# Kernel optimization log

Hardware: AMD Instinct MI355X
Metric: run time of the kernel (lower is better)

## Reference

```python
import jax, jax.numpy as jnp
import numpy as np
import math

H = 8
D_MODEL = 512
D_K = D_MODEL // H
DIM_G = 64
WAVE_LEN = 1000.0


def box_relational_embedding(f_g):
    # f_g: [B, N, 4] -> [B, N, N, 64] trigonometric geometry embedding
    x_min, y_min, x_max, y_max = jnp.split(f_g, 4, axis=-1)  # each [B,N,1]
    cx = (x_min + x_max) * 0.5
    cy = (y_min + y_max) * 0.5
    w = x_max - x_min + 1.0
    h = y_max - y_min + 1.0
    # pairwise deltas: [B,N,1] vs [B,1,N] -> [B,N,N]
    cx_t = jnp.swapaxes(cx, 1, 2)  # [B,1,N]
    cy_t = jnp.swapaxes(cy, 1, 2)
    w_t = jnp.swapaxes(w, 1, 2)
    h_t = jnp.swapaxes(h, 1, 2)
    delta_x = jnp.log(jnp.maximum(jnp.abs((cx - cx_t) / w), 0.001))
    delta_y = jnp.log(jnp.maximum(jnp.abs((cy - cy_t) / h), 0.001))
    delta_w = jnp.log(w / w_t)
    delta_h = jnp.log(h / h_t)
    position_mat = jnp.stack([delta_x, delta_y, delta_w, delta_h], axis=-1)  # [B,N,N,4]
    feat_range = jnp.arange(DIM_G // 8, dtype=position_mat.dtype) / (DIM_G / 8)
    dim_mat = 1.0 / jnp.power(jnp.asarray(WAVE_LEN, position_mat.dtype), feat_range)  # [8]
    mul_mat = (100.0 * position_mat)[..., None] * dim_mat  # [B,N,N,4,8]
    B, N = position_mat.shape[0], position_mat.shape[1]
    mul_mat = mul_mat.reshape(B, N, N, -1)  # [B,N,N,32]
    return jnp.concatenate([jnp.sin(mul_mat), jnp.cos(mul_mat)], axis=-1)  # [B,N,N,64]


def setup_inputs() -> dict:
    key = jax.random.key(0)
    ks = jax.random.split(key, 16)
    B, N = 16, 256
    scale = 1.0 / math.sqrt(D_MODEL)
    inp = {
        'input_query': jax.random.normal(ks[0], (B, N, D_MODEL), jnp.float32),
        'input_key': jax.random.normal(ks[1], (B, N, D_MODEL), jnp.float32),
        'input_value': jax.random.normal(ks[2], (B, N, D_MODEL), jnp.float32),
        'input_box': jax.random.uniform(ks[3], (B, N, 4), jnp.float32),
        'mask': jnp.ones((B, N), jnp.int32),
        # projection weights stored as [d_in, d_out] (x @ W + b)
        'Wq': jax.random.normal(ks[4], (D_MODEL, D_MODEL), jnp.float32) * scale,
        'bq': jnp.zeros((D_MODEL,), jnp.float32),
        'Wk': jax.random.normal(ks[5], (D_MODEL, D_MODEL), jnp.float32) * scale,
        'bk': jnp.zeros((D_MODEL,), jnp.float32),
        'Wv': jax.random.normal(ks[6], (D_MODEL, D_MODEL), jnp.float32) * scale,
        'bv': jnp.zeros((D_MODEL,), jnp.float32),
        'Wo': jax.random.normal(ks[7], (D_MODEL, D_MODEL), jnp.float32) * scale,
        'bo': jnp.zeros((D_MODEL,), jnp.float32),
        # 8 geometric-bias heads: Linear(64 -> 1) each, stacked -> [H, 64], [H]
        'WG_w': jax.random.normal(ks[8], (H, DIM_G), jnp.float32) * (1.0 / math.sqrt(DIM_G)),
        'WG_b': jnp.zeros((H,), jnp.float32),
    }
    return inp


def reference(input_query, input_key, input_value, input_box, mask,
              Wq, bq, Wk, bk, Wv, bv, Wo, bo, WG_w, WG_b):
    B, N, _ = input_query.shape

    def proj(x, W, b):  # [B,N,D] -> [B,H,N,d_k]
        return (x @ W + b).reshape(B, N, H, D_K).transpose(0, 2, 1, 3)

    q = proj(input_query, Wq, bq)
    k = proj(input_key, Wk, bk)
    v = proj(input_value, Wv, bv)

    geo = box_relational_embedding(input_box)  # [B,N,N,64]
    # per-head geometric weights, ReLU'd: [B,H,N,N]
    w_g = jax.nn.relu(jnp.einsum('bnmg,hg->bhnm', geo, WG_w) + WG_b[None, :, None, None])

    scaled_dot = jnp.einsum('bhqd,bhkd->bhqk', q, k) / np.sqrt(D_K).astype(q.dtype)
    # mask: [B,N] keys -> [B,1,1,N], broadcast over heads and queries
    scaled_dot = jnp.where(mask[:, None, None, :] == 0, jnp.asarray(-1e9, scaled_dot.dtype), scaled_dot)
    w_mn = jax.nn.softmax(jnp.log(jnp.maximum(w_g, 1e-6)) + scaled_dot, axis=-1)
    # dropout is identity in eval mode
    out = jnp.einsum('bhqk,bhkd->bhqd', w_mn, v)  # [B,H,N,d_k]
    out = out.transpose(0, 2, 1, 3).reshape(B, N, H * D_K)
    return out @ Wo + bo
```

## Files before the change

### kernel.cpp

```cpp
#include <hip/hip_runtime.h>
#include <hip/hip_fp16.h>
#include <math.h>

#define Bv   16
#define Nv   256
#define Dv   512
#define Hv   8
#define MNv  4096

typedef __attribute__((ext_vector_type(8))) short bf16x8;
typedef __attribute__((ext_vector_type(4))) float f32x4;
typedef __fp16 fp16x8 __attribute__((ext_vector_type(8)));
typedef __fp16 fp16x2 __attribute__((ext_vector_type(2)));

__device__ __forceinline__ unsigned short f2bf(float f) {
    unsigned u = __float_as_uint(f);
    u = u + 0x7FFFu + ((u >> 16) & 1u);
    return (unsigned short)(u >> 16);
}
__device__ __forceinline__ void gload_lds16(const void* g, void* l) {
    __builtin_amdgcn_global_load_lds(
        (const __attribute__((address_space(1))) unsigned int*)g,
        (__attribute__((address_space(3))) unsigned int*)l, 16, 0, 0);
}

__device__ __forceinline__ void fast_sincos(float x, float* s, float* c) {
    const float rev = x * 0.15915494309189535f;
    const float fr  = rev - floorf(rev);
    *s = __builtin_amdgcn_sinf(fr);
    *c = __builtin_amdgcn_cosf(fr);
}
__device__ __forceinline__ float fast_log(float x) {
    return __builtin_amdgcn_logf(x) * 0.6931471805599453f;
}
__device__ __forceinline__ float fast_exp(float x) {
    return __builtin_amdgcn_exp2f(x * 1.4426950408889634f);
}

__global__ __launch_bounds__(256) void mega1_kernel(
    const float* __restrict__ box, const int* __restrict__ mask,
    const float* __restrict__ WGw, const float* __restrict__ WGb,
    __half* __restrict__ LB,
    const float* __restrict__ xq, const float* __restrict__ xk,
    const float* __restrict__ xv, unsigned short* __restrict__ Ab,
    const float* __restrict__ Wq, const float* __restrict__ Wk,
    const float* __restrict__ Wv, const float* __restrict__ Wo,
    const float* __restrict__ bq, const float* __restrict__ bk,
    const float* __restrict__ bv, const float* __restrict__ bo,
    unsigned short* __restrict__ Wt, float* __restrict__ biasStack)
{
    __shared__ __align__(16) char smraw[64 * 65 * 4];
    const int bid = blockIdx.x;
    const int t = threadIdx.x;

    if (bid < 4096) {
        unsigned short (*Lst)[264] = (unsigned short (*)[264])smraw;
        const int q = bid & 255;
        const int b = bid >> 8;
        const int w = t >> 6, lane = t & 63;
        const int n = lane & 15;
        const int quad = lane >> 4;

        const float4 bq_ = *(const float4*)(box + (b * Nv + q) * 4);
        const float cxq = (bq_.x + bq_.z) * 0.5f;
        const float cyq = (bq_.y + bq_.w) * 0.5f;
        const float wq  = bq_.z - bq_.x + 1.0f;
        const float hq  = bq_.w - bq_.y + 1.0f;

        union F16x8 { fp16x8 v; fp16x2 p[4]; };
        F16x8 Bs_, Bc_;
        Bs_.v = (fp16x8){}; Bc_.v = (fp16x8){};
        float bias_n = 0.0f;
        if (n < Hv) {
            bias_n = WGb[n];
#pragma unroll
            for (int jj = 0; jj < 4; ++jj) {
                Bs_.p[jj] = __builtin_amdgcn_cvt_pkrtz(WGw[n * 64 + quad * 8 + 2 * jj],
                                                       WGw[n * 64 + quad * 8 + 2 * jj + 1]);
                Bc_.p[jj] = __builtin_amdgcn_cvt_pkrtz(WGw[n * 64 + 32 + quad * 8 + 2 * jj],
                                                       WGw[n * 64 + 32 + quad * 8 + 2 * jj + 1]);
            }
        }

        const float dimm[8] = {1.0f, 0.42169650342f, 0.17782794100f, 0.07498942093f,
                               0.03162277660f, 0.01333521432f, 0.00562341325f, 0.00237137371f};
        const bool isCtr = (quad < 2);
        const bool isY   = (quad & 1);
        const float cq  = isY ? cyq : cxq;
        const float sq_ = isY ? hq : wq;

#pragma unroll
        for (int i = 0; i < 4; ++i) {
            const int m0 = (w * 4 + i) * 16;
            const float4 bm = *(const float4*)(box + (b * Nv + m0 + n) * 4);
            const float cxm = (bm.x + bm.z) * 0.5f;
            const float cym = (bm.y + bm.w) * 0.5f;
            const float wm  = bm.z - bm.x + 1.0f;
            const float hm  = bm.w - bm.y + 1.0f;
            const float cm_ = isY ? cym : cxm;
            const float sm_ = isY ? hm : wm;
            const float top = isCtr ? fabsf(cq - cm_) : sq_;
            const float bot = isCtr ? sq_ : sm_;
            float r = top * __builtin_amdgcn_rcpf(bot);
            if (isCtr) r = fmaxf(r, 1e-3f);
            const float base = 69.31471805599453f * __builtin_amdgcn_logf(r);

            float sv[8], cv[8];
#pragma unroll
            for (int j = 0; j < 8; ++j)
                fast_sincos(base * dimm[j], &sv[j], &cv[j]);

            F16x8 As_, Ac_;
#pragma unroll
            for (int jj = 0; jj < 4; ++jj) {
                As_.p[jj] = __builtin_amdgcn_cvt_pkrtz(sv[2 * jj], sv[2 * jj + 1]);
                Ac_.p[jj] = __builtin_amdgcn_cvt_pkrtz(cv[2 * jj], cv[2 * jj + 1]);
            }

            f32x4 acc = {};
            acc = __builtin_amdgcn_mfma_f32_16x16x32_f16(As_.v, Bs_.v, acc, 0, 0, 0);
            acc = __builtin_amdgcn_mfma_f32_16x16x32_f16(Ac_.v, Bc_.v, acc, 0, 0, 0);

            const int mrow = m0 + quad * 4;
            const int4 mk = *(const int4*)(mask + b * Nv + mrow);
            if (n < Hv) {
                const int* mkp = (const int*)&mk;
                const int pos0 = quad * 64 + (w * 4 + i);
#pragma unroll
                for (int rr = 0; rr < 4; ++rr) {
                    const float val = fmaxf(acc[rr] + bias_n, 1e-6f);
                    const float lb = fast_log(val) + (mkp[rr] ? 0.0f : -30000.0f);
                    Lst[n][pos0 + rr * 16] = __half_as_ushort(__float2half(lb));
                }
            }
        }

        __syncthreads();
        const int h = t >> 5, c = t & 31;
        unsigned short* dst = (unsigned short*)LB +
                              ((size_t)(b * Hv + h) * Nv + q) * Nv + c * 8;
        *(int4*)dst = *(const int4*)&Lst[h][c * 8];

    } else if (bid < 10240) {
        const int i = bid - 4096;
        const int z = i >> 11;
        const int xblk = i & 2047;
        const float* src = (z == 0) ? xq : (z == 1) ? xk : xv;
        const size_t base = (size_t)z * (MNv * Dv);
        const int idx = (xblk * 256 + t) * 4;
        float4 x = *(const float4*)(src + idx);
        ushort4 h4;
        h4.x = f2bf(x.x); h4.y = f2bf(x.y); h4.z = f2bf(x.z); h4.w = f2bf(x.w);
        *(ushort4*)(Ab + base + idx) = h4;

    } else {
        float (*T)[65] = (float (*)[65])smraw;
        const int i = bid - 10240;
        const int z = i >> 6;
        const int rem = i & 63;
        const int n0 = (rem & 7) * 64, k0 = (rem >> 3) * 64;
        const float* W = (z == 0) ? Wq : (z == 1) ? Wk : (z == 2) ? Wv : Wo;
        const float* b = (z == 0) ? bq : (z == 1) ? bk : (z == 2) ? bv : bo;
        const int col = t & 63, rb = t >> 6;
#pragma unroll
        for (int j = 0; j < 16; ++j) {
            const int row = j * 4 + rb;
            T[row][col] = W[(k0 + row) * Dv + n0 + col];
        }
        __syncthreads();
#pragma unroll
        for (int j = 0; j < 16; ++j) {
            const int row = j * 4 + rb;
            Wt[z * (Dv * Dv) + (n0 + row) * Dv + k0 + col] = f2bf(T[col][row]);
        }
        if (rem == 0) {
            biasStack[z * Dv + t]       = b[t];
            biasStack[z * Dv + t + 256] = b[t + 256];
        }
    }
}

__global__ __launch_bounds__(256) void qkv_gemm_kernel(
    const unsigned short* __restrict__ Ab, const unsigned short* __restrict__ Wt,
    const float* __restrict__ bst, unsigned short* __restrict__ Qb2,
    unsigned short* __restrict__ Kb2, unsigned short* __restrict__ Vt2)
{
    const int z = blockIdx.z;
    const unsigned short* A = Ab + (size_t)z * (MNv * Dv);
    const unsigned short* Wz = Wt + (size_t)z * (Dv * Dv);
    const float* bias = bst + z * Dv;

    const int n0 = blockIdx.x * 64;
    const int m0 = blockIdx.y * 128;
    const int t = threadIdx.x;
    const int w = t >> 6, lane = t & 63;
    const int wm = w & 1, wn = w >> 1;

    __shared__ __align__(16) unsigned short As[2][2][128][32];
    __shared__ __align__(16) unsigned short Bs[2][2][64][32];

    f32x4 acc[4][2] = {};

    const int sr = t >> 2;
    const int sc = (t & 3) * 8;
    const int fr = lane & 15;
    const int fq = lane >> 4;

    auto STAGE = [&](int bu, int k0) {
#pragma unroll
        for (int kk = 0; kk < 2; ++kk) {
#pragma unroll
            for (int i = 0; i < 2; ++i)
                gload_lds16(A + (size_t)(m0 + i * 64 + sr) * Dv + k0 + kk * 32 + sc,
                            &As[bu][kk][i * 64 + w * 16][0]);
            gload_lds16(Wz + (size_t)(n0 + sr) * Dv + k0 + kk * 32 + sc,
                        &Bs[bu][kk][w * 16][0]);
        }
    };

    STAGE(0, 0);
    __syncthreads();
    int cur = 0;
#pragma unroll
    for (int kt = 0; kt < 8; ++kt) {
        if (kt < 7) STAGE(cur ^ 1, (kt + 1) * 64);

        bf16x8 af[2][4], bfr[2][2];
#pragma unroll
        for (int kk = 0; kk < 2; ++kk) {
#pragma unroll
            for (int mt = 0; mt < 4; ++mt)
                af[kk][mt] = *(const bf16x8*)&As[cur][kk][wm * 64 + mt * 16 + fr][fq * 8];
#pragma unroll
            for (int nt = 0; nt < 2; ++nt)
                bfr[kk][nt] = *(const bf16x8*)&Bs[cur][kk][wn * 32 + nt * 16 + fr][fq * 8];
        }
#pragma unroll
        for (int mt = 0; mt < 4; ++mt)
#pragma unroll
            for (int nt = 0; nt < 2; ++nt) {
                acc[mt][nt] = __builtin_amdgcn_mfma_f32_16x16x32_bf16(
                    af[0][mt], bfr[0][nt], acc[mt][nt], 0, 0, 0);
                acc[mt][nt] = __builtin_amdgcn_mfma_f32_16x16x32_bf16(
                    af[1][mt], bfr[1][nt], acc[mt][nt], 0, 0, 0);
            }
        __syncthreads();
        cur ^= 1;
    }

    const int er = (lane >> 4) * 4;
    const int ec = lane & 15;
    const float scale = (z == 0) ? 0.125f : 1.0f;
#pragma unroll
    for (int nt = 0; nt < 2; ++nt) {
        const int gn = n0 + wn * 32 + nt * 16 + ec;
        const float bv_ = bias[gn];
#pragma unroll
        for (int mt = 0; mt < 4; ++mt) {
            const int gm = m0 + wm * 64 + mt * 16 + er;
            if (z == 2) {
                ushort4 o;
                o.x = f2bf(acc[mt][nt][0] + bv_);
                o.y = f2bf(acc[mt][nt][1] + bv_);
                o.z = f2bf(acc[mt][nt][2] + bv_);
                o.w = f2bf(acc[mt][nt][3] + bv_);
                *(ushort4*)(Vt2 + ((size_t)(gm >> 8) * Dv + gn) * Nv + (gm & 255)) = o;
            } else {
                unsigned short* cp = ((z == 0) ? Qb2 : Kb2) + (size_t)gm * Dv + gn;
#pragma unroll
                for (int r = 0; r < 4; ++r)
                    cp[(size_t)r * Dv] = f2bf((acc[mt][nt][r] + bv_) * scale);
            }
        }
    }
}

__global__ __launch_bounds__(256) void out_gemm_kernel(
    const unsigned short* __restrict__ A, const unsigned short* __restrict__ Wz,
    const float* __restrict__ bias, float* __restrict__ C)
{
    const int n0 = blockIdx.x * 64;
    const int m0 = blockIdx.y * 128;
    const int t = threadIdx.x;
    const int w = t >> 6, lane = t & 63;
    const int wm = w & 1, wn = w >> 1;

    __shared__ __align__(16) unsigned short As[2][2][128][32];
    __shared__ __align__(16) unsigned short Bs[2][2][64][32];

    f32x4 acc[4][2] = {};

    const int sr = t >> 2;
    const int sc = (t & 3) * 8;
    const int fr = lane & 15;
    const int fq = lane >> 4;

    auto STAGE = [&](int bu, int k0) {
#pragma unroll
        for (int kk = 0; kk < 2; ++kk) {
#pragma unroll
            for (int i = 0; i < 2; ++i)
                gload_lds16(A + (size_t)(m0 + i * 64 + sr) * Dv + k0 + kk * 32 + sc,
                            &As[bu][kk][i * 64 + w * 16][0]);
            gload_lds16(Wz + (size_t)(n0 + sr) * Dv + k0 + kk * 32 + sc,
                        &Bs[bu][kk][w * 16][0]);
        }
    };

    STAGE(0, 0);
    __syncthreads();
    int cur = 0;
#pragma unroll
    for (int kt = 0; kt < 8; ++kt) {
        if (kt < 7) STAGE(cur ^ 1, (kt + 1) * 64);

        bf16x8 af[2][4], bfr[2][2];
#pragma unroll
        for (int kk = 0; kk < 2; ++kk) {
#pragma unroll
            for (int mt = 0; mt < 4; ++mt)
                af[kk][mt] = *(const bf16x8*)&As[cur][kk][wm * 64 + mt * 16 + fr][fq * 8];
#pragma unroll
            for (int nt = 0; nt < 2; ++nt)
                bfr[kk][nt] = *(const bf16x8*)&Bs[cur][kk][wn * 32 + nt * 16 + fr][fq * 8];
        }
#pragma unroll
        for (int mt = 0; mt < 4; ++mt)
#pragma unroll
            for (int nt = 0; nt < 2; ++nt) {
                acc[mt][nt] = __builtin_amdgcn_mfma_f32_16x16x32_bf16(
                    af[0][mt], bfr[0][nt], acc[mt][nt], 0, 0, 0);
                acc[mt][nt] = __builtin_amdgcn_mfma_f32_16x16x32_bf16(
                    af[1][mt], bfr[1][nt], acc[mt][nt], 0, 0, 0);
            }
        __syncthreads();
        cur ^= 1;
    }

    const int er = (lane >> 4) * 4;
    const int ec = lane & 15;
#pragma unroll
    for (int nt = 0; nt < 2; ++nt) {
        const int gn = n0 + wn * 32 + nt * 16 + ec;
        const float bv_ = bias[gn];
#pragma unroll
        for (int mt = 0; mt < 4; ++mt) {
            const int gm = m0 + wm * 64 + mt * 16 + er;
            float* cp = C + (size_t)gm * Dv + gn;
#pragma unroll
            for (int r = 0; r < 4; ++r)
                cp[(size_t)r * Dv] = acc[mt][nt][r] + bv_;
        }
    }
}

__global__ __launch_bounds__(256) void attn3_kernel(
    const unsigned short* __restrict__ Qb2, const unsigned short* __restrict__ Kb2,
    const unsigned short* __restrict__ Vt2, const __half* __restrict__ LB,
    unsigned short* __restrict__ CTXb)
{
    const int qt = blockIdx.x, h = blockIdx.y, b = blockIdx.z;
    const int q0 = qt * 64;
    const int t = threadIdx.x, w = t >> 6, lane = t & 63;
    const int fr = lane & 15, fq = lane >> 4;

    __shared__ __align__(16) unsigned short smem[36864];
    unsigned short (*K0)[32] = (unsigned short (*)[32])&smem[0];
    unsigned short (*K1)[32] = (unsigned short (*)[32])&smem[8192];
    unsigned short (*Q0)[32] = (unsigned short (*)[32])&smem[16384];
    unsigned short (*Q1)[32] = (unsigned short (*)[32])&smem[18432];
    unsigned short (*Vs)[32] = (unsigned short (*)[32])&smem[20480];
    unsigned short (*Pb)[264] = (unsigned short (*)[264])&smem[0];

    const int sr = t >> 2;
    const int sc = (t & 3) * 8;

    const int qb = q0 + w * 16 + fq * 4;
    const __half* lbp = LB + ((size_t)(b * Hv + h) * Nv + qb) * Nv + fr * 16;
    int4 lbv[4][2];
#pragma unroll
    for (int r = 0; r < 4; ++r) {
        const int4* p = (const int4*)(lbp + (size_t)r * Nv);
        lbv[r][0] = p[0];
        lbv[r][1] = p[1];
    }

#pragma unroll
    for (int i = 0; i < 4; ++i) {
        gload_lds16(Kb2 + (size_t)(b * Nv + i * 64 + sr) * Dv + h * 64 + sc,
                    &K0[i * 64 + w * 16][0]);
        gload_lds16(Kb2 + (size_t)(b * Nv + i * 64 + sr) * Dv + h * 64 + 32 + sc,
                    &K1[i * 64 + w * 16][0]);
    }
    gload_lds16(Qb2 + (size_t)(b * Nv + q0 + sr) * Dv + h * 64 + sc,
                &Q0[w * 16][0]);
    gload_lds16(Qb2 + (size_t)(b * Nv + q0 + sr) * Dv + h * 64 + 32 + sc,
                &Q1[w * 16][0]);
#pragma unroll
    for (int kt = 0; kt < 8; ++kt)
        gload_lds16(Vt2 + (size_t)b * (Dv * Nv) + (h * 64 + sr) * Nv + kt * 32 + sc,
                    &Vs[kt * 64 + w * 16][0]);

    f32x4 acc[16];
#pragma unroll
    for (int r = 0; r < 4; ++r) {
        const __half* hs0 = (const __half*)&lbv[r][0];
        const __half* hs1 = (const __half*)&lbv[r][1];
#pragma unroll
        for (int nt = 0; nt < 8; ++nt) acc[nt][r]     = __half2float(hs0[nt]);
#pragma unroll
        for (int nt = 0; nt < 8; ++nt) acc[nt + 8][r] = __half2float(hs1[nt]);
    }

    __syncthreads();

    const bf16x8 aq0 = *(const bf16x8*)&Q0[w * 16 + fr][fq * 8];
    const bf16x8 aq1 = *(const bf16x8*)&Q1[w * 16 + fr][fq * 8];
#pragma unroll
    for (int nt = 0; nt < 16; ++nt) {
        const bf16x8 bk0 = *(const bf16x8*)&K0[nt * 16 + fr][fq * 8];
        const bf16x8 bk1 = *(const bf16x8*)&K1[nt * 16 + fr][fq * 8];
        acc[nt] = __builtin_amdgcn_mfma_f32_16x16x32_bf16(aq0, bk0, acc[nt], 0, 0, 0);
        acc[nt] = __builtin_amdgcn_mfma_f32_16x16x32_bf16(aq1, bk1, acc[nt], 0, 0, 0);
    }

    float ri[4];
#pragma unroll
    for (int r = 0; r < 4; ++r) {
        float mx = acc[0][r];
#pragma unroll
        for (int nt = 1; nt < 16; ++nt) mx = fmaxf(mx, acc[nt][r]);
        mx = fmaxf(mx, __shfl_xor(mx, 1));
        mx = fmaxf(mx, __shfl_xor(mx, 2));
        mx = fmaxf(mx, __shfl_xor(mx, 4));
        mx = fmaxf(mx, __shfl_xor(mx, 8));
        float s = 0.0f;
#pragma unroll
        for (int nt = 0; nt < 16; ++nt) {
            const float e = fast_exp(acc[nt][r] - mx);
            acc[nt][r] = e;
            s += e;
        }
        s += __shfl_xor(s, 1);
        s += __shfl_xor(s, 2);
        s += __shfl_xor(s, 4);
        s += __shfl_xor(s, 8);
        ri[r] = __builtin_amdgcn_rcpf(s);
    }

    __syncthreads();

#pragma unroll
    for (int nt = 0; nt < 16; ++nt)
#pragma unroll
        for (int r = 0; r < 4; ++r)
            Pb[w * 16 + fq * 4 + r][nt * 16 + fr] = f2bf(acc[nt][r] * ri[r]);

    f32x4 o[4] = {};
#pragma unroll
    for (int kt = 0; kt < 8; ++kt) {
        const bf16x8 ap = *(const bf16x8*)&Pb[w * 16 + fr][kt * 32 + fq * 8];
#pragma unroll
        for (int nt2 = 0; nt2 < 4; ++nt2) {
            const bf16x8 bv_ = *(const bf16x8*)&Vs[kt * 64 + nt2 * 16 + fr][fq * 8];
            o[nt2] = __builtin_amdgcn_mfma_f32_16x16x32_bf16(ap, bv_, o[nt2], 0, 0, 0);
        }
    }

#pragma unroll
    for (int nt2 = 0; nt2 < 4; ++nt2)
#pragma unroll
        for (int r = 0; r < 4; ++r)
            CTXb[(size_t)(b * Nv + qb + r) * Dv + h * 64 + nt2 * 16 + fr] =
                f2bf(o[nt2][r]);
}

extern "C" void kernel_launch(void* const* d_in, const int* in_sizes, int n_in,
                              void* d_out, int out_size, void* d_ws, size_t ws_size,
                              hipStream_t stream) {
    (void)in_sizes; (void)n_in; (void)out_size; (void)ws_size;

    const float* inq  = (const float*)d_in[0];
    const float* ink  = (const float*)d_in[1];
    const float* inv  = (const float*)d_in[2];
    const float* box  = (const float*)d_in[3];
    const int*   mask = (const int*)d_in[4];
    const float* Wq   = (const float*)d_in[5];
    const float* bq   = (const float*)d_in[6];
    const float* Wk   = (const float*)d_in[7];
    const float* bk   = (const float*)d_in[8];
    const float* Wv   = (const float*)d_in[9];
    const float* bv   = (const float*)d_in[10];
    const float* Wo   = (const float*)d_in[11];
    const float* bo   = (const float*)d_in[12];
    const float* WGw  = (const float*)d_in[13];
    const float* WGb  = (const float*)d_in[14];

    char* W = (char*)d_ws;
    const size_t MB = 1048576;
    unsigned short* Qb2  = (unsigned short*)(W + 0);
    unsigned short* Kb2  = (unsigned short*)(W + 4 * MB);
    unsigned short* Vt2  = (unsigned short*)(W + 8 * MB);
    unsigned short* Wt   = (unsigned short*)(W + 12 * MB);
    float*          bst  = (float*)(W + 14 * MB);
    unsigned short* CTXb = (unsigned short*)(W + 15 * MB);
    unsigned short* Ab   = (unsigned short*)(W + 20 * MB);
    __half*         LB   = (__half*)(W + 32 * MB);

    float* out = (float*)d_out;

    mega1_kernel<<<10496, 256, 0, stream>>>(
        box, mask, WGw, WGb, LB,
        inq, ink, inv, Ab,
        Wq, Wk, Wv, Wo, bq, bk, bv, bo, Wt, bst);

    qkv_gemm_kernel<<<dim3(8, 32, 3), 256, 0, stream>>>(Ab, Wt, bst, Qb2, Kb2, Vt2);

    attn3_kernel<<<dim3(4, 8, 16), 256, 0, stream>>>(Qb2, Kb2, Vt2, LB, CTXb);

    out_gemm_kernel<<<dim3(8, 32), 256, 0, stream>>>(CTXb, Wt + 3 * (Dv * Dv), bst + 3 * Dv, out);
}
```

Before: 157.0 us.

## Fuse all four stages into one cooperative persistent kernel with grid syncs

Replaces the four separate launches (prep, QKV GEMM, attention, output GEMM) with a single cooperative kernel of 512 blocks that walks through the stages, separated by grid-wide barriers. Each block now handles multiple work items per stage (12 conversion chunks, 8 query rows of geometry bias, one or two GEMM tiles). The aim is to remove per-launch overhead and inter-kernel gaps. In exchange, grid.sync costs are added, parallelism drops to 512 blocks (the QKV stage becomes imbalanced, with half the blocks doing two tiles), and launch_bounds(256,2) may constrain registers.

Result: slower. 507.3 us (+223.1%).

```diff
diff --git a/kernel.cpp b/kernel.cpp
--- a/kernel.cpp
+++ b/kernel.cpp
@@ -1,6 +1,9 @@
 #include <hip/hip_runtime.h>
+#include <hip/hip_cooperative_groups.h>
 #include <hip/hip_fp16.h>
 #include <math.h>
+
+namespace cg = cooperative_groups;
 
 #define Bv   16
 #define Nv   256
@@ -23,7 +26,6 @@
         (const __attribute__((address_space(1))) unsigned int*)g,
         (__attribute__((address_space(3))) unsigned int*)l, 16, 0, 0);
 }
-
 __device__ __forceinline__ void fast_sincos(float x, float* s, float* c) {
     const float rev = x * 0.15915494309189535f;
     const float fr  = rev - floorf(rev);
@@ -37,35 +39,50 @@
     return __builtin_amdgcn_exp2f(x * 1.4426950408889634f);
 }
 
-__global__ __launch_bounds__(256) void mega1_kernel(
+__global__ __launch_bounds__(256, 2) void fused_kernel(
     const float* __restrict__ box, const int* __restrict__ mask,
     const float* __restrict__ WGw, const float* __restrict__ WGb,
-    __half* __restrict__ LB,
     const float* __restrict__ xq, const float* __restrict__ xk,
-    const float* __restrict__ xv, unsigned short* __restrict__ Ab,
+    const float* __restrict__ xv,
     const float* __restrict__ Wq, const float* __restrict__ Wk,
     const float* __restrict__ Wv, const float* __restrict__ Wo,
     const float* __restrict__ bq, const float* __restrict__ bk,
     const float* __restrict__ bv, const float* __restrict__ bo,
-    unsigned short* __restrict__ Wt, float* __restrict__ biasStack)
+    unsigned short* __restrict__ Ab, unsigned short* __restrict__ Wt,
+    float* __restrict__ bst, __half* __restrict__ LB,
+    unsigned short* __restrict__ Qb2, unsigned short* __restrict__ Kb2,
+    unsigned short* __restrict__ Vt2, unsigned short* __restrict__ CTXb,
+    float* __restrict__ out)
 {
-    __shared__ __align__(16) char smraw[64 * 65 * 4];
+    cg::grid_group grid = cg::this_grid();
+    __shared__ __align__(16) unsigned short smem[36864];
+
     const int bid = blockIdx.x;
     const int t = threadIdx.x;
-
-    if (bid < 4096) {
-        unsigned short (*Lst)[264] = (unsigned short (*)[264])smraw;
-        const int q = bid & 255;
-        const int b = bid >> 8;
-        const int w = t >> 6, lane = t & 63;
+    const int w = t >> 6, lane = t & 63;
+
+    {
+#pragma unroll
+        for (int k = 0; k < 12; ++k) {
+            const int u = bid * 12 + k;
+            const int z = u >> 11;
+            const int xblk = u & 2047;
+            const float* src = (z == 0) ? xq : (z == 1) ? xk : xv;
+            const size_t base = (size_t)z * (MNv * Dv);
+            const int idx = (xblk * 256 + t) * 4;
+            float4 x = *(const float4*)(src + idx);
+            ushort4 h4;
+            h4.x = f2bf(x.x); h4.y = f2bf(x.y); h4.z = f2bf(x.z); h4.w = f2bf(x.w);
+            *(ushort4*)(Ab + base + idx) = h4;
+        }
+    }
+
+    {
+        unsigned short (*Lst)[264] = (unsigned short (*)[264])smem;
         const int n = lane & 15;
         const int quad = lane >> 4;
-
-        const float4 bq_ = *(const float4*)(box + (b * Nv + q) * 4);
-        const float cxq = (bq_.x + bq_.z) * 0.5f;
-        const float cyq = (bq_.y + bq_.w) * 0.5f;
-        const float wq  = bq_.z - bq_.x + 1.0f;
-        const float hq  = bq_.w - bq_.y + 1.0f;
+        const int b = bid >> 5;
+        const int q0u = (bid & 31) * 8;
 
         union F16x8 { fp16x8 v; fp16x2 p[4]; };
         F16x8 Bs_, Bc_;
@@ -86,9 +103,9 @@
                                0.03162277660f, 0.01333521432f, 0.00562341325f, 0.00237137371f};
         const bool isCtr = (quad < 2);
         const bool isY   = (quad & 1);
-        const float cq  = isY ? cyq : cxq;
-        const float sq_ = isY ? hq : wq;
-
+
+        float cmv[4], smv[4];
+        int4 mkv[4];
 #pragma unroll
         for (int i = 0; i < 4; ++i) {
             const int m0 = (w * 4 + i) * 16;
@@ -97,70 +114,74 @@
             const float cym = (bm.y + bm.w) * 0.5f;
             const float wm  = bm.z - bm.x + 1.0f;
             const float hm  = bm.w - bm.y + 1.0f;
-            const float cm_ = isY ? cym : cxm;
-            const float sm_ = isY ? hm : wm;
-            const float top = isCtr ? fabsf(cq - cm_) : sq_;
-            const float bot = isCtr ? sq_ : sm_;
-            float r = top * __builtin_amdgcn_rcpf(bot);
-            if (isCtr) r = fmaxf(r, 1e-3f);
-            const float base = 69.31471805599453f * __builtin_amdgcn_logf(r);
-
-            float sv[8], cv[8];
-#pragma unroll
-            for (int j = 0; j < 8; ++j)
-                fast_sincos(base * dimm[j], &sv[j], &cv[j]);
-
-            F16x8 As_, Ac_;
-#pragma unroll
-            for (int jj = 0; jj < 4; ++jj) {
-                As_.p[jj] = __builtin_amdgcn_cvt_pkrtz(sv[2 * jj], sv[2 * jj + 1]);
-                Ac_.p[jj] = __builtin_amdgcn_cvt_pkrtz(cv[2 * jj], cv[2 * jj + 1]);
-            }
-
-            f32x4 acc = {};
-            acc = __builtin_amdgcn_mfma_f32_16x16x32_f16(As_.v, Bs_.v, acc, 0, 0, 0);
-            acc = __builtin_amdgcn_mfma_f32_16x16x32_f16(Ac_.v, Bc_.v, acc, 0, 0, 0);
-
-            const int mrow = m0 + quad * 4;
-            const int4 mk = *(const int4*)(mask + b * Nv + mrow);
-            if (n < Hv) {
-                const int* mkp = (const int*)&mk;
-                const int pos0 = quad * 64 + (w * 4 + i);
-#pragma unroll
-                for (int rr = 0; rr < 4; ++rr) {
-                    const float val = fmaxf(acc[rr] + bias_n, 1e-6f);
-                    const float lb = fast_log(val) + (mkp[rr] ? 0.0f : -30000.0f);
-                    Lst[n][pos0 + rr * 16] = __half_as_ushort(__float2half(lb));
+            cmv[i] = isY ? cym : cxm;
+            smv[i] = isY ? hm : wm;
+            mkv[i] = *(const int4*)(mask + b * Nv + m0 + quad * 4);
+        }
+
+#pragma unroll 1
+        for (int k = 0; k < 8; ++k) {
+            const int q = q0u + k;
+            const float4 bq_ = *(const float4*)(box + (b * Nv + q) * 4);
+            const float cxq = (bq_.x + bq_.z) * 0.5f;
+            const float cyq = (bq_.y + bq_.w) * 0.5f;
+            const float wq_ = bq_.z - bq_.x + 1.0f;
+            const float hq_ = bq_.w - bq_.y + 1.0f;
+            const float cq  = isY ? cyq : cxq;
+            const float sq2 = isY ? hq_ : wq_;
+
+#pragma unroll
+            for (int i = 0; i < 4; ++i) {
+                const float top = isCtr ? fabsf(cq - cmv[i]) : sq2;
+                const float bot = isCtr ? sq2 : smv[i];
+                float r = top * __builtin_amdgcn_rcpf(bot);
+                if (isCtr) r = fmaxf(r, 1e-3f);
+                const float base = 69.31471805599453f * __builtin_amdgcn_logf(r);
+
+                float sv[8], cv[8];
+#pragma unroll
+                for (int j = 0; j < 8; ++j)
+                    fast_sincos(base * dimm[j], &sv[j], &cv[j]);
+
+                F16x8 As_, Ac_;
+#pragma unroll
+                for (int jj = 0; jj < 4; ++jj) {
+                    As_.p[jj] = __builtin_amdgcn_cvt_pkrtz(sv[2 * jj], sv[2 * jj + 1]);
+                    Ac_.p[jj] = __builtin_amdgcn_cvt_pkrtz(cv[2 * jj], cv[2 * jj + 1]);
                 }
-            }
-        }
-
-        __syncthreads();
-        const int h = t >> 5, c = t & 31;
-        unsigned short* dst = (unsigned short*)LB +
-                              ((size_t)(b * Hv + h) * Nv + q) * Nv + c * 8;
-        *(int4*)dst = *(const int4*)&Lst[h][c * 8];
-
-    } else if (bid < 10240) {
-        const int i = bid - 4096;
-        const int z = i >> 11;
-        const int xblk = i & 2047;
-        const float* src = (z == 0) ? xq : (z == 1) ? xk : xv;
-        const size_t base = (size_t)z * (MNv * Dv);
-        const int idx = (xblk * 256 + t) * 4;
-        float4 x = *(const float4*)(src + idx);
-        ushort4 h4;
-        h4.x = f2bf(x.x); h4.y = f2bf(x.y); h4.z = f2bf(x.z); h4.w = f2bf(x.w);
-        *(ushort4*)(Ab + base + idx) = h4;
-
-    } else {
-        float (*T)[65] = (float (*)[65])smraw;
-        const int i = bid - 10240;
-        const int z = i >> 6;
-        const int rem = i & 63;
+
+                f32x4 acc = {};
+                acc = __builtin_amdgcn_mfma_f32_16x16x32_f16(As_.v, Bs_.v, acc, 0, 0, 0);
+                acc = __builtin_amdgcn_mfma_f32_16x16x32_f16(Ac_.v, Bc_.v, acc, 0, 0, 0);
+
+                if (n < Hv) {
+                    const int* mkp = (const int*)&mkv[i];
+                    const int pos0 = quad * 64 + (w * 4 + i);
+#pragma unroll
+                    for (int rr = 0; rr < 4; ++rr) {
+                        const float val = fmaxf(acc[rr] + bias_n, 1e-6f);
+                        const float lb = fast_log(val) + (mkp[rr] ? 0.0f : -30000.0f);
+                        Lst[n][pos0 + rr * 16] = __half_as_ushort(__float2half(lb));
+                    }
+                }
+            }
+
+            __syncthreads();
+            const int hh = t >> 5, c = t & 31;
+            unsigned short* dst = (unsigned short*)LB +
+                                  ((size_t)(b * Hv + hh) * Nv + q) * Nv + c * 8;
+            *(int4*)dst = *(const int4*)&Lst[hh][c * 8];
+            __syncthreads();
+        }
+    }
+
+    if (bid < 256) {
+        float (*T)[65] = (float (*)[65])smem;
+        const int z = bid >> 6;
+        const int rem = bid & 63;
         const int n0 = (rem & 7) * 64, k0 = (rem >> 3) * 64;
         const float* W = (z == 0) ? Wq : (z == 1) ? Wk : (z == 2) ? Wv : Wo;
-        const float* b = (z == 0) ? bq : (z == 1) ? bk : (z == 2) ? bv : bo;
+        const float* b2 = (z == 0) ? bq : (z == 1) ? bk : (z == 2) ? bv : bo;
         const int col = t & 63, rb = t >> 6;
 #pragma unroll
         for (int j = 0; j < 16; ++j) {
@@ -174,305 +195,288 @@
             Wt[z * (Dv * Dv) + (n0 + row) * Dv + k0 + col] = f2bf(T[col][row]);
         }
         if (rem == 0) {
-            biasStack[z * Dv + t]       = b[t];
-            biasStack[z * Dv + t + 256] = b[t + 256];
+            bst[z * Dv + t]       = b2[t];
+            bst[z * Dv + t + 256] = b2[t + 256];
         }
     }
-}
-
-__global__ __launch_bounds__(256) void qkv_gemm_kernel(
-    const unsigned short* __restrict__ Ab, const unsigned short* __restrict__ Wt,
-    const float* __restrict__ bst, unsigned short* __restrict__ Qb2,
-    unsigned short* __restrict__ Kb2, unsigned short* __restrict__ Vt2)
-{
-    const int z = blockIdx.z;
-    const unsigned short* A = Ab + (size_t)z * (MNv * Dv);
-    const unsigned short* Wz = Wt + (size_t)z * (Dv * Dv);
-    const float* bias = bst + z * Dv;
-
-    const int n0 = blockIdx.x * 64;
-    const int m0 = blockIdx.y * 128;
-    const int t = threadIdx.x;
-    const int w = t >> 6, lane = t & 63;
-    const int wm = w & 1, wn = w >> 1;
-
-    __shared__ __align__(16) unsigned short As[2][2][128][32];
-    __shared__ __align__(16) unsigned short Bs[2][2][64][32];
-
-    f32x4 acc[4][2] = {};
-
-    const int sr = t >> 2;
-    const int sc = (t & 3) * 8;
-    const int fr = lane & 15;
-    const int fq = lane >> 4;
-
-    auto STAGE = [&](int bu, int k0) {
-#pragma unroll
-        for (int kk = 0; kk < 2; ++kk) {
-#pragma unroll
-            for (int i = 0; i < 2; ++i)
-                gload_lds16(A + (size_t)(m0 + i * 64 + sr) * Dv + k0 + kk * 32 + sc,
-                            &As[bu][kk][i * 64 + w * 16][0]);
-            gload_lds16(Wz + (size_t)(n0 + sr) * Dv + k0 + kk * 32 + sc,
-                        &Bs[bu][kk][w * 16][0]);
-        }
-    };
-
-    STAGE(0, 0);
-    __syncthreads();
-    int cur = 0;
-#pragma unroll
-    for (int kt = 0; kt < 8; ++kt) {
-        if (kt < 7) STAGE(cur ^ 1, (kt + 1) * 64);
-
-        bf16x8 af[2][4], bfr[2][2];
-#pragma unroll
-        for (int kk = 0; kk < 2; ++kk) {
-#pragma unroll
-            for (int mt = 0; mt < 4; ++mt)
-                af[kk][mt] = *(const bf16x8*)&As[cur][kk][wm * 64 + mt * 16 + fr][fq * 8];
-#pragma unroll
-            for (int nt = 0; nt < 2; ++nt)
-                bfr[kk][nt] = *(const bf16x8*)&Bs[cur][kk][wn * 32 + nt * 16 + fr][fq * 8];
-        }
-#pragma unroll
-        for (int mt = 0; mt < 4; ++mt)
+
+    __threadfence();
+    grid.sync();
+
+    {
+        const int sr = t >> 2;
+        const int sc = (t & 3) * 8;
+        const int fr = lane & 15;
+        const int fq = lane >> 4;
+        const int wm = w & 1, wn = w >> 1;
+
+        auto qkv_tile = [&](int tile) {
+            const int z = tile >> 8;
+            const int rem = tile & 255;
+            const int n0 = (rem & 7) * 64;
+            const int m0 = (rem >> 3) * 128;
+            const unsigned short* A = Ab + (size_t)z * (MNv * Dv);
+            const unsigned short* Wz = Wt + (size_t)z * (Dv * Dv);
+            const float* bias = bst + z * Dv;
+
+            f32x4 acc[4][2] = {};
+            auto STAGE = [&](int bu, int k0) {
+#pragma unroll
+                for (int kk = 0; kk < 2; ++kk) {
+#pragma unroll
+                    for (int i2 = 0; i2 < 2; ++i2)
+                        gload_lds16(A + (size_t)(m0 + i2 * 64 + sr) * Dv + k0 + kk * 32 + sc,
+                                    &smem[((bu * 2 + kk) * 128 + i2 * 64 + w * 16) * 32]);
+                    gload_lds16(Wz + (size_t)(n0 + sr) * Dv + k0 + kk * 32 + sc,
+                                &smem[16384 + ((bu * 2 + kk) * 64 + w * 16) * 32]);
+                }
+            };
+
+            STAGE(0, 0);
+            __syncthreads();
+            int cur = 0;
+#pragma unroll
+            for (int kt = 0; kt < 8; ++kt) {
+                if (kt < 7) STAGE(cur ^ 1, (kt + 1) * 64);
+                bf16x8 af[2][4], bfr[2][2];
+#pragma unroll
+                for (int kk = 0; kk < 2; ++kk) {
+#pragma unroll
+                    for (int mt = 0; mt < 4; ++mt)
+                        af[kk][mt] = *(const bf16x8*)
+                            &smem[((cur * 2 + kk) * 128 + wm * 64 + mt * 16 + fr) * 32 + fq * 8];
+#pragma unroll
+                    for (int nt = 0; nt < 2; ++nt)
+                        bfr[kk][nt] = *(const bf16x8*)
+                            &smem[16384 + ((cur * 2 + kk) * 64 + wn * 32 + nt * 16 + fr) * 32 + fq * 8];
+                }
+#pragma unroll
+                for (int mt = 0; mt < 4; ++mt)
+#pragma unroll
+                    for (int nt = 0; nt < 2; ++nt) {
+                        acc[mt][nt] = __builtin_amdgcn_mfma_f32_16x16x32_bf16(
+                            af[0][mt], bfr[0][nt], acc[mt][nt], 0, 0, 0);
+                        acc[mt][nt] = __builtin_amdgcn_mfma_f32_16x16x32_bf16(
+                            af[1][mt], bfr[1][nt], acc[mt][nt], 0, 0, 0);
+                    }
+                __syncthreads();
+                cur ^= 1;
+            }
+
+            const int er = (lane >> 4) * 4;
+            const int ec = lane & 15;
+            const float scale = (z == 0) ? 0.125f : 1.0f;
 #pragma unroll
             for (int nt = 0; nt < 2; ++nt) {
-                acc[mt][nt] = __builtin_amdgcn_mfma_f32_16x16x32_bf16(
-                    af[0][mt], bfr[0][nt], acc[mt][nt], 0, 0, 0);
-                acc[mt][nt] = __builtin_amdgcn_mfma_f32_16x16x32_bf16(
-                    af[1][mt], bfr[1][nt], acc[mt][nt], 0, 0, 0);
-            }
+                const int gn = n0 + wn * 32 + nt * 16 + ec;
+                const float bv_ = bias[gn];
+#pragma unroll
+                for (int mt = 0; mt < 4; ++mt) {
+                    const int gm = m0 + wm * 64 + mt * 16 + er;
+                    if (z == 2) {
+                        ushort4 o;
+                        o.x = f2bf(acc[mt][nt][0] + bv_);
+                        o.y = f2bf(acc[mt][nt][1] + bv_);
+                        o.z = f2bf(acc[mt][nt][2] + bv_);
+                        o.w = f2bf(acc[mt][nt][3] + bv_);
+                        *(ushort4*)(Vt2 + ((size_t)(gm >> 8) * Dv + gn) * Nv + (gm & 255)) = o;
+                    } else {
+                        unsigned short* cp = ((z == 0) ? Qb2 : Kb2) + (size_t)gm * Dv + gn;
+#pragma unroll
+                        for (int r = 0; r < 4; ++r)
+                            cp[(size_t)r * Dv] = f2bf((acc[mt][nt][r] + bv_) * scale);
+                    }
+                }
+            }
+        };
+
+        qkv_tile(bid);
         __syncthreads();
-        cur ^= 1;
+        if (bid < 256) qkv_tile(bid + 512);
     }
 
-    const int er = (lane >> 4) * 4;
-    const int ec = lane & 15;
-    const float scale = (z == 0) ? 0.125f : 1.0f;
-#pragma unroll
-    for (int nt = 0; nt < 2; ++nt) {
-        const int gn = n0 + wn * 32 + nt * 16 + ec;
-        const float bv_ = bias[gn];
-#pragma unroll
-        for (int mt = 0; mt < 4; ++mt) {
-            const int gm = m0 + wm * 64 + mt * 16 + er;
-            if (z == 2) {
-                ushort4 o;
-                o.x = f2bf(acc[mt][nt][0] + bv_);
-                o.y = f2bf(acc[mt][nt][1] + bv_);
-                o.z = f2bf(acc[mt][nt][2] + bv_);
-                o.w = f2bf(acc[mt][nt][3] + bv_);
-                *(ushort4*)(Vt2 + ((size_t)(gm >> 8) * Dv + gn) * Nv + (gm & 255)) = o;
-            } else {
-                unsigned short* cp = ((z == 0) ? Qb2 : Kb2) + (size_t)gm * Dv + gn;
-#pragma unroll
-                for (int r = 0; r < 4; ++r)
-                    cp[(size_t)r * Dv] = f2bf((acc[mt][nt][r] + bv_) * scale);
-            }
-        }
+    __threadfence();
+    grid.sync();
+
+    {
+        const int qt = bid & 3, h = (bid >> 2) & 7, b = bid >> 5;
+        const int q0 = qt * 64;
+        const int fr = lane & 15, fq = lane >> 4;
+
+        unsigned short (*K0)[32] = (unsigned short (*)[32])&smem[0];
+        unsigned short (*K1)[32] = (unsigned short (*)[32])&smem[8192];
+        unsigned short (*Q0)[32] = (unsigned short (*)[32])&smem[16384];
+        unsigned short (*Q1)[32] = (unsigned short (*)[32])&smem[18432];
+        unsigned short (*Vs)[32] = (unsigned short (*)[32])&smem[20480];
+        unsigned short (*Pb)[264] = (unsigned short (*)[264])&smem[0];
+
+        const int sr = t >> 2;
+        const int sc = (t & 3) * 8;
+
+        const int qb = q0 + w * 16 + fq * 4;
+        const __half* lbp = LB + ((size_t)(b * Hv + h) * Nv + qb) * Nv + fr * 16;
+        int4 lbv[4][2];
+#pragma unroll
+        for (int r = 0; r < 4; ++r) {
+            const int4* p = (const int4*)(lbp + (size_t)r * Nv);
+            lbv[r][0] = p[0];
+            lbv[r][1] = p[1];
+        }
+
+#pragma unroll
+        for (int i = 0; i < 4; ++i) {
+            gload_lds16(Kb2 + (size_t)(b * Nv + i * 64 + sr) * Dv + h * 64 + sc,
+                        &K0[i * 64 + w * 16][0]);
+            gload_lds16(Kb2 + (size_t)(b * Nv + i * 64 + sr) * Dv + h * 64 + 32 + sc,
+                        &K1[i * 64 + w * 16][0]);
+        }
+        gload_lds16(Qb2 + (size_t)(b * Nv + q0 + sr) * Dv + h * 64 + sc, &Q0[w * 16][0]);
+        gload_lds16(Qb2 + (size_t)(b * Nv + q0 + sr) * Dv + h * 64 + 32 + sc, &Q1[w * 16][0]);
+#pragma unroll
+        for (int kt = 0; kt < 8; ++kt)
+            gload_lds16(Vt2 + (size_t)b * (Dv * Nv) + (h * 64 + sr) * Nv + kt * 32 + sc,
+                        &Vs[kt * 64 + w * 16][0]);
+
+        f32x4 acc[16];
+#pragma unroll
+        for (int r = 0; r < 4; ++r) {
+            const __half* hs0 = (const __half*)&lbv[r][0];
+            const __half* hs1 = (const __half*)&lbv[r][1];
+#pragma unroll
+            for (int nt = 0; nt < 8; ++nt) acc[nt][r]     = __half2float(hs0[nt]);
+#pragma unroll
+            for (int nt = 0; nt < 8; ++nt) acc[nt + 8][r] = __half2float(hs1[nt]);
+        }
+
+        __syncthreads();
+
+        const bf16x8 aq0 = *(const bf16x8*)&Q0[w * 16 + fr][fq * 8];
+        const bf16x8 aq1 = *(const bf16x8*)&Q1[w * 16 + fr][fq * 8];
+#pragma unroll
+        for (int nt = 0; nt < 16; ++nt) {
+            const bf16x8 bk0 = *(const bf16x8*)&K0[nt * 16 + fr][fq * 8];
+            const bf16x8 bk1 = *(const bf16x8*)&K1[nt * 16 + fr][fq * 8];
+            acc[nt] = __builtin_amdgcn_mfma_f32_16x16x32_bf16(aq0, bk0, acc[nt], 0, 0, 0);
+            acc[nt] = __builtin_amdgcn_mfma_f32_16x16x32_bf16(aq1, bk1, acc[nt], 0, 0, 0);
+        }
+
+        float ri[4];
+#pragma unroll
+        for (int r = 0; r < 4; ++r) {
+            float mx = acc[0][r];
+#pragma unroll
+            for (int nt = 1; nt < 16; ++nt) mx = fmaxf(mx, acc[nt][r]);
+            mx = fmaxf(mx, __shfl_xor(mx, 1));
+            mx = fmaxf(mx, __shfl_xor(mx, 2));
+            mx = fmaxf(mx, __shfl_xor(mx, 4));
+            mx = fmaxf(mx, __shfl_xor(mx, 8));
+            float s = 0.0f;
+#pragma unroll
+            for (int nt = 0; nt < 16; ++nt) {
+                const float e = fast_exp(acc[nt][r] - mx);
+                acc[nt][r] = e;
+                s += e;
+            }
+            s += __shfl_xor(s, 1);
+            s += __shfl_xor(s, 2);
+            s += __shfl_xor(s, 4);
+            s += __shfl_xor(s, 8);
+            ri[r] = __builtin_amdgcn_rcpf(s);
+        }
+
+        __syncthreads();
+
+#pragma unroll
+        for (int nt = 0; nt < 16; ++nt)
+#pragma unroll
+            for (int r = 0; r < 4; ++r)
+                Pb[w * 16 + fq * 4 + r][nt * 16 + fr] = f2bf(acc[nt][r] * ri[r]);
+
+        f32x4 o[4] = {};
+#pragma unroll
+        for (int kt = 0; kt < 8; ++kt) {
+            const bf16x8 ap = *(const bf16x8*)&Pb[w * 16 + fr][kt * 32 + fq * 8];
+#pragma unroll
+            for (int nt2 = 0; nt2 < 4; ++nt2) {
+                const bf16x8 bv_ = *(const bf16x8*)&Vs[kt * 64 + nt2 * 16 + fr][fq * 8];
+                o[nt2] = __builtin_amdgcn_mfma_f32_16x16x32_bf16(ap, bv_, o[nt2], 0, 0, 0);
+            }
+        }
+
+#pragma unroll
+        for (int nt2 = 0; nt2 < 4; ++nt2)
+#pragma unroll
+            for (int r = 0; r < 4; ++r)
+                CTXb[(size_t)(b * Nv + qb + r) * Dv + h * 64 + nt2 * 16 + fr] =
+                    f2bf(o[nt2][r]);
+
+        __syncthreads();
     }
-}
-
-__global__ __launch_bounds__(256) void out_gemm_kernel(
-    const unsigned short* __restrict__ A, const unsigned short* __restrict__ Wz,
-    const float* __restrict__ bias, float* __restrict__ C)
-{
-    const int n0 = blockIdx.x * 64;
-    const int m0 = blockIdx.y * 128;
-    const int t = threadIdx.x;
-    const int w = t >> 6, lane = t & 63;
-    const int wm = w & 1, wn = w >> 1;
-
-    __shared__ __align__(16) unsigned short As[2][2][128][32];
-    __shared__ __align__(16) unsigned short Bs[2][2][64][32];
-
-    f32x4 acc[4][2] = {};
-
-    const int sr = t >> 2;
-    const int sc = (t & 3) * 8;
-    const int fr = lane & 15;
-    const int fq = lane >> 4;
-
-    auto STAGE = [&](int bu, int k0) {
-#pragma unroll
-        for (int kk = 0; kk < 2; ++kk) {
-#pragma unroll
-            for (int i = 0; i < 2; ++i)
-                gload_lds16(A + (size_t)(m0 + i * 64 + sr) * Dv + k0 + kk * 32 + sc,
-                            &As[bu][kk][i * 64 + w * 16][0]);
-            gload_lds16(Wz + (size_t)(n0 + sr) * Dv + k0 + kk * 32 + sc,
-                        &Bs[bu][kk][w * 16][0]);
-        }
-    };
-
-    STAGE(0, 0);
-    __syncthreads();
-    int cur = 0;
-#pragma unroll
-    for (int kt = 0; kt < 8; ++kt) {
-        if (kt < 7) STAGE(cur ^ 1, (kt + 1) * 64);
-
-        bf16x8 af[2][4], bfr[2][2];
-#pragma unroll
-        for (int kk = 0; kk < 2; ++kk) {
-#pragma unroll
-            for (int mt = 0; mt < 4; ++mt)
-                af[kk][mt] = *(const bf16x8*)&As[cur][kk][wm * 64 + mt * 16 + fr][fq * 8];
-#pragma unroll
-            for (int nt = 0; nt < 2; ++nt)
-                bfr[kk][nt] = *(const bf16x8*)&Bs[cur][kk][wn * 32 + nt * 16 + fr][fq * 8];
-        }
-#pragma unroll
-        for (int mt = 0; mt < 4; ++mt)
-#pragma unroll
-            for (int nt = 0; nt < 2; ++nt) {
-                acc[mt][nt] = __builtin_amdgcn_mfma_f32_16x16x32_bf16(
-                    af[0][mt], bfr[0][nt], acc[mt][nt], 0, 0, 0);
-                acc[mt][nt] = __builtin_amdgcn_mfma_f32_16x16x32_bf16(
-                    af[1][mt], bfr[1][nt], acc[mt][nt], 0, 0, 0);
-            }
+
+    __threadfence();
+    grid.sync();
+
+    {
+        const int n0 = (bid & 7) * 64;
+        const int m0 = (bid >> 3) * 64;
+        const int sr = t >> 2;
+        const int sc = (t & 3) * 8;
+        const int fr = lane & 15;
+        const int fq = lane >> 4;
+        const unsigned short* Wzo = Wt + 3 * (Dv * Dv);
+        const float* biaso = bst + 3 * Dv;
+
+        f32x4 acc[4] = {};
+        auto STG = [&](int bu, int k0) {
+#pragma unroll
+            for (int kk = 0; kk < 2; ++kk) {
+                gload_lds16(CTXb + (size_t)(m0 + sr) * Dv + k0 + kk * 32 + sc,
+                            &smem[((bu * 2 + kk) * 64 + w * 16) * 32]);
+                gload_lds16(Wzo + (size_t)(n0 + sr) * Dv + k0 + kk * 32 + sc,
+                            &smem[8192 + ((bu * 2 + kk) * 64 + w * 16) * 32]);
+            }
+        };
+
+        STG(0, 0);
         __syncthreads();
-        cur ^= 1;
+        int cur = 0;
+#pragma unroll
+        for (int kt = 0; kt < 8; ++kt) {
+            if (kt < 7) STG(cur ^ 1, (kt + 1) * 64);
+            bf16x8 af[2];
+            bf16x8 bfr[2][4];
+#pragma unroll
+            for (int kk = 0; kk < 2; ++kk) {
+                af[kk] = *(const bf16x8*)
+                    &smem[((cur * 2 + kk) * 64 + w * 16 + fr) * 32 + fq * 8];
+#pragma unroll
+                for (int nt = 0; nt < 4; ++nt)
+                    bfr[kk][nt] = *(const bf16x8*)
+                        &smem[8192 + ((cur * 2 + kk) * 64 + nt * 16 + fr) * 32 + fq * 8];
+            }
+#pragma unroll
+            for (int nt = 0; nt < 4; ++nt) {
+                acc[nt] = __builtin_amdgcn_mfma_f32_16x16x32_bf16(
+                    af[0], bfr[0][nt], acc[nt], 0, 0, 0);
+                acc[nt] = __builtin_amdgcn_mfma_f32_16x16x32_bf16(
+                    af[1], bfr[1][nt], acc[nt], 0, 0, 0);
+            }
+            __syncthreads();
+            cur ^= 1;
+        }
+
+        const int er = (lane >> 4) * 4;
+        const int ec = lane & 15;
+#pragma unroll
+        for (int nt = 0; nt < 4; ++nt) {
+            const int gn = n0 + nt * 16 + ec;
+            const float bv_ = biaso[gn];
+            float* cp = out + (size_t)(m0 + w * 16 + er) * Dv + gn;
+#pragma unroll
+            for (int r = 0; r < 4; ++r)
+                cp[(size_t)r * Dv] = acc[nt][r] + bv_;
+        }
     }
-
-    const int er = (lane >> 4) * 4;
-    const int ec = lane & 15;
-#pragma unroll
-    for (int nt = 0; nt < 2; ++nt) {
-        const int gn = n0 + wn * 32 + nt * 16 + ec;
-        const float bv_ = bias[gn];
-#pragma unroll
-        for (int mt = 0; mt < 4; ++mt) {
-            const int gm = m0 + wm * 64 + mt * 16 + er;
-            float* cp = C + (size_t)gm * Dv + gn;
-#pragma unroll
-            for (int r = 0; r < 4; ++r)
-                cp[(size_t)r * Dv] = acc[mt][nt][r] + bv_;
-        }
-    }
-}
-
-__global__ __launch_bounds__(256) void attn3_kernel(
-    const unsigned short* __restrict__ Qb2, const unsigned short* __restrict__ Kb2,
-    const unsigned short* __restrict__ Vt2, const __half* __restrict__ LB,
-    unsigned short* __restrict__ CTXb)
-{
-    const int qt = blockIdx.x, h = blockIdx.y, b = blockIdx.z;
-    const int q0 = qt * 64;
-    const int t = threadIdx.x, w = t >> 6, lane = t & 63;
-    const int fr = lane & 15, fq = lane >> 4;
-
-    __shared__ __align__(16) unsigned short smem[36864];
-    unsigned short (*K0)[32] = (unsigned short (*)[32])&smem[0];
-    unsigned short (*K1)[32] = (unsigned short (*)[32])&smem[8192];
-    unsigned short (*Q0)[32] = (unsigned short (*)[32])&smem[16384];
-    unsigned short (*Q1)[32] = (unsigned short (*)[32])&smem[18432];
-    unsigned short (*Vs)[32] = (unsigned short (*)[32])&smem[20480];
-    unsigned short (*Pb)[264] = (unsigned short (*)[264])&smem[0];
-
-    const int sr = t >> 2;
-    const int sc = (t & 3) * 8;
-
-    const int qb = q0 + w * 16 + fq * 4;
-    const __half* lbp = LB + ((size_t)(b * Hv + h) * Nv + qb) * Nv + fr * 16;
-    int4 lbv[4][2];
-#pragma unroll
-    for (int r = 0; r < 4; ++r) {
-        const int4* p = (const int4*)(lbp + (size_t)r * Nv);
-        lbv[r][0] = p[0];
-        lbv[r][1] = p[1];
-    }
-
-#pragma unroll
-    for (int i = 0; i < 4; ++i) {
-        gload_lds16(Kb2 + (size_t)(b * Nv + i * 64 + sr) * Dv + h * 64 + sc,
-                    &K0[i * 64 + w * 16][0]);
-        gload_lds16(Kb2 + (size_t)(b * Nv + i * 64 + sr) * Dv + h * 64 + 32 + sc,
-                    &K1[i * 64 + w * 16][0]);
-    }
-    gload_lds16(Qb2 + (size_t)(b * Nv + q0 + sr) * Dv + h * 64 + sc,
-                &Q0[w * 16][0]);
-    gload_lds16(Qb2 + (size_t)(b * Nv + q0 + sr) * Dv + h * 64 + 32 + sc,
-                &Q1[w * 16][0]);
-#pragma unroll
-    for (int kt = 0; kt < 8; ++kt)
-        gload_lds16(Vt2 + (size_t)b * (Dv * Nv) + (h * 64 + sr) * Nv + kt * 32 + sc,
-                    &Vs[kt * 64 + w * 16][0]);
-
-    f32x4 acc[16];
-#pragma unroll
-    for (int r = 0; r < 4; ++r) {
-        const __half* hs0 = (const __half*)&lbv[r][0];
-        const __half* hs1 = (const __half*)&lbv[r][1];
-#pragma unroll
-        for (int nt = 0; nt < 8; ++nt) acc[nt][r]     = __half2float(hs0[nt]);
-#pragma unroll
-        for (int nt = 0; nt < 8; ++nt) acc[nt + 8][r] = __half2float(hs1[nt]);
-    }
-
-    __syncthreads();
-
-    const bf16x8 aq0 = *(const bf16x8*)&Q0[w * 16 + fr][fq * 8];
-    const bf16x8 aq1 = *(const bf16x8*)&Q1[w * 16 + fr][fq * 8];
-#pragma unroll
-    for (int nt = 0; nt < 16; ++nt) {
-        const bf16x8 bk0 = *(const bf16x8*)&K0[nt * 16 + fr][fq * 8];
-        const bf16x8 bk1 = *(const bf16x8*)&K1[nt * 16 + fr][fq * 8];
-        acc[nt] = __builtin_amdgcn_mfma_f32_16x16x32_bf16(aq0, bk0, acc[nt], 0, 0, 0);
-        acc[nt] = __builtin_amdgcn_mfma_f32_16x16x32_bf16(aq1, bk1, acc[nt], 0, 0, 0);
-    }
-
-    float ri[4];
-#pragma unroll
-    for (int r = 0; r < 4; ++r) {
-        float mx = acc[0][r];
-#pragma unroll
-        for (int nt = 1; nt < 16; ++nt) mx = fmaxf(mx, acc[nt][r]);
-        mx = fmaxf(mx, __shfl_xor(mx, 1));
-        mx = fmaxf(mx, __shfl_xor(mx, 2));
-        mx = fmaxf(mx, __shfl_xor(mx, 4));
-        mx = fmaxf(mx, __shfl_xor(mx, 8));
-        float s = 0.0f;
-#pragma unroll
-        for (int nt = 0; nt < 16; ++nt) {
-            const float e = fast_exp(acc[nt][r] - mx);
-            acc[nt][r] = e;
-            s += e;
-        }
-        s += __shfl_xor(s, 1);
-        s += __shfl_xor(s, 2);
-        s += __shfl_xor(s, 4);
-        s += __shfl_xor(s, 8);
-        ri[r] = __builtin_amdgcn_rcpf(s);
-    }
-
-    __syncthreads();
-
-#pragma unroll
-    for (int nt = 0; nt < 16; ++nt)
-#pragma unroll
-        for (int r = 0; r < 4; ++r)
-            Pb[w * 16 + fq * 4 + r][nt * 16 + fr] = f2bf(acc[nt][r] * ri[r]);
-
-    f32x4 o[4] = {};
-#pragma unroll
-    for (int kt = 0; kt < 8; ++kt) {
-        const bf16x8 ap = *(const bf16x8*)&Pb[w * 16 + fr][kt * 32 + fq * 8];
-#pragma unroll
-        for (int nt2 = 0; nt2 < 4; ++nt2) {
-            const bf16x8 bv_ = *(const bf16x8*)&Vs[kt * 64 + nt2 * 16 + fr][fq * 8];
-            o[nt2] = __builtin_amdgcn_mfma_f32_16x16x32_bf16(ap, bv_, o[nt2], 0, 0, 0);
-        }
-    }
-
-#pragma unroll
-    for (int nt2 = 0; nt2 < 4; ++nt2)
-#pragma unroll
-        for (int r = 0; r < 4; ++r)
-            CTXb[(size_t)(b * Nv + qb + r) * Dv + h * 64 + nt2 * 16 + fr] =
-                f2bf(o[nt2][r]);
 }
 
 extern "C" void kernel_launch(void* const* d_in, const int* in_sizes, int n_in,
@@ -509,14 +513,14 @@
 
     float* out = (float*)d_out;
 
-    mega1_kernel<<<10496, 256, 0, stream>>>(
-        box, mask, WGw, WGb, LB,
-        inq, ink, inv, Ab,
-        Wq, Wk, Wv, Wo, bq, bk, bv, bo, Wt, bst);
-
-    qkv_gemm_kernel<<<dim3(8, 32, 3), 256, 0, stream>>>(Ab, Wt, bst, Qb2, Kb2, Vt2);
-
-    attn3_kernel<<<dim3(4, 8, 16), 256, 0, stream>>>(Qb2, Kb2, Vt2, LB, CTXb);
-
-    out_gemm_kernel<<<dim3(8, 32), 256, 0, stream>>>(CTXb, Wt + 3 * (Dv * Dv), bst + 3 * Dv, out);
-}
+    void* args[] = {
+        (void*)&box, (void*)&mask, (void*)&WGw, (void*)&WGb,
+        (void*)&inq, (void*)&ink, (void*)&inv,
+        (void*)&Wq, (void*)&Wk, (void*)&Wv, (void*)&Wo,
+        (void*)&bq, (void*)&bk, (void*)&bv, (void*)&bo,
+        (void*)&Ab, (void*)&Wt, (void*)&bst, (void*)&LB,
+        (void*)&Qb2, (void*)&Kb2, (void*)&Vt2, (void*)&CTXb, (void*)&out
+    };
+    hipLaunchCooperativeKernel(reinterpret_cast<void*>(fused_kernel),
+                               dim3(512), dim3(256), args, 0, stream);
+}
```
